# Optimization experiments

Hardware: AMD Instinct MI355X
Metric: run time of the kernel (lower is better)

## Reference

```python
import jax, jax.numpy as jnp
import numpy as np

NUM_HEADS = 16
H_SELF = 10  # hardcoded h in forward: first 10 heads self-attend, rest cross-attend
DIM = 1024
HEAD_DIM = DIM // NUM_HEADS
SCALE = HEAD_DIM ** -0.5


def _qkv(x, Wqkv):
    # x: [B, N, C] -> q, k, v each [B, H, N, hd]
    B, N, C = x.shape
    qkv = (x @ Wqkv).reshape(B, N, 3, NUM_HEADS, C // NUM_HEADS).transpose(2, 0, 3, 1, 4)
    return qkv[0], qkv[1], qkv[2]


def _attn(q, k, v):
    # q,k,v: [B, h, N, d]
    scores = jnp.einsum('bhqd,bhkd->bhqk', q, k) * SCALE
    probs = jax.nn.softmax(scores, axis=-1)  # attn_drop_ratio = 0.0
    return jnp.einsum('bhqk,bhkd->bhqd', probs, v)


def _proj(xa, xb, Wproj, bproj):
    # xa: [B, 10, N, d], xb: [B, 6, N, d] -> [B, N, C]
    B = xa.shape[0]
    N = xa.shape[2]
    x = jnp.concatenate([xa, xb], axis=1).transpose(0, 2, 1, 3).reshape(B, N, DIM)
    return x @ Wproj + bproj  # proj_drop_ratio = 0.0


def setup_inputs() -> dict:
    key = jax.random.key(0)
    k0, k1, k2, k3 = jax.random.split(key, 4)
    B, N, C = 16, 577, DIM
    x1 = jax.random.normal(k0, (B, N, C), dtype=jnp.float32)
    x2 = jax.random.normal(k1, (B, N, C), dtype=jnp.float32)
    # nn.Linear(dim, dim*3, bias=False): store as [C, 3C] so y = x @ W
    Wqkv = jax.random.normal(k2, (C, 3 * C), dtype=jnp.float32) * 0.02
    # nn.Linear(dim, dim) has bias by default
    Wproj = jax.random.normal(k3, (C, C), dtype=jnp.float32) * 0.02
    bproj = jnp.zeros((C,), dtype=jnp.float32)
    return {"x1": x1, "x2": x2, "Wqkv": Wqkv, "Wproj": Wproj, "bproj": bproj}


def reference(x1, x2, Wqkv, Wproj, bproj):
    q1, k1, v1 = _qkv(x1, Wqkv)
    q2, k2, v2 = _qkv(x2, Wqkv)
    h = H_SELF
    x11 = _attn(q1[:, :h], k1[:, :h], v1[:, :h])  # self-attn branch of x1
    x12 = _attn(q1[:, h:], k2[:, h:], v2[:, h:])  # cross: q from x1, kv from x2
    x22 = _attn(q2[:, :h], k2[:, :h], v2[:, :h])  # self-attn branch of x2
    x21 = _attn(q2[:, h:], k1[:, h:], v1[:, h:])  # cross: q from x2, kv from x1
    out1 = _proj(x11, x12, Wproj, bproj)
    out2 = _proj(x22, x21, Wproj, bproj)
    return (out1, out2)
```

## Files before the change

### kernel.cpp

```cpp
#include <hip/hip_runtime.h>
#include <hip/hip_bf16.h>
#include <stdint.h>
#include <math.h>

typedef __attribute__((ext_vector_type(8))) short bf16x8;
typedef __attribute__((ext_vector_type(4))) float f32x4;
typedef __attribute__((ext_vector_type(8))) unsigned short ushort8;
typedef __attribute__((ext_vector_type(4))) unsigned int uint4v;
typedef __attribute__((ext_vector_type(2))) unsigned int uint2v;

#define NTOK   9232
#define MROWS  18464
#define MPAD   18560
#define NPADV  640
#define QSCALE 0.18033688011112042f

__device__ __forceinline__ uint16_t f2b(float f) {
  uint32_t u = __builtin_bit_cast(uint32_t, f);
  u += 0x7fffu + ((u >> 16) & 1u);
  return (uint16_t)(u >> 16);
}

__device__ __forceinline__ uint32_t packbf(float lo, float hi) {
  return (uint32_t)f2b(lo) | ((uint32_t)f2b(hi) << 16);
}

__device__ __forceinline__ f32x4 mfma16(bf16x8 a, bf16x8 b, f32x4 c) {
  return __builtin_amdgcn_mfma_f32_16x16x32_bf16(a, b, c, 0, 0, 0);
}

__device__ __forceinline__ void gl_lds16(const void* g, void* l) {
  __builtin_amdgcn_global_load_lds(
      (const __attribute__((address_space(1))) uint32_t*)g,
      (__attribute__((address_space(3))) uint32_t*)l, 16, 0, 0);
}

__global__ void convert_x_kernel(const float* __restrict__ x1,
                                 const float* __restrict__ x2,
                                 uint16_t* __restrict__ Xb) {
  const size_t stride = (size_t)gridDim.x * blockDim.x;
  const size_t total8 = (size_t)MPAD * 1024 / 8;
  for (size_t i = (size_t)blockIdx.x * blockDim.x + threadIdx.x; i < total8; i += stride) {
    const size_t e = i * 8;
    const size_t row = e >> 10;
    ushort8 ov;
    if (row < (size_t)MROWS) {
      const float* src = (row < (size_t)NTOK) ? (x1 + e) : (x2 + (e - (size_t)NTOK * 1024));
      float4 a = *(const float4*)(src);
      float4 b = *(const float4*)(src + 4);
      ov[0] = f2b(a.x); ov[1] = f2b(a.y); ov[2] = f2b(a.z); ov[3] = f2b(a.w);
      ov[4] = f2b(b.x); ov[5] = f2b(b.y); ov[6] = f2b(b.z); ov[7] = f2b(b.w);
    } else {
      ov = (ushort8)0;
    }
    *(ushort8*)(Xb + e) = ov;
  }
}

__global__ void transw_kernel(const float* __restrict__ in, uint16_t* __restrict__ out,
                              int R, int Cc) {
  __shared__ float t[32][33];
  const int r0 = blockIdx.x * 32, c0 = blockIdx.y * 32;
  const int tr = threadIdx.x >> 5, tc = threadIdx.x & 31;
#pragma unroll
  for (int i = 0; i < 4; ++i)
    t[tr + i * 8][tc] = in[(size_t)(r0 + tr + i * 8) * Cc + c0 + tc];
  __syncthreads();
#pragma unroll
  for (int i = 0; i < 4; ++i) {
    const int orow = c0 + tr + i * 8;
    out[(size_t)orow * R + r0 + tc] = f2b(t[tc][tr + i * 8]);
  }
}

__global__ void zero_vpad_kernel(uint16_t* __restrict__ Vtb) {
  const int idx = blockIdx.x * 256 + threadIdx.x;
  for (int i = idx; i < 32768 * 8; i += 256 * 256) {
    const int p = i >> 3;
    const int ch = i & 7;
    *(ushort8*)(Vtb + (size_t)p * NPADV + 576 + ch * 8) = (ushort8)0;
  }
}

#define GEMM_TRI_SETUP                                                         \
  const int srow4 = tt >> 2;                                        \
  const int schunk = tt & 3;                         \
  const int swc = schunk ^ ((srow4 >> 1) & 3);                                 \
  const int crs = (c >> 1) & 3;                                                \
  char* aL = (char*)As3;                                                       \
  char* bL = (char*)Bs3;                                                       \
  auto SA = [&](int buf, int t) {                                              \
    _Pragma("unroll")                                                          \
    for (int i = 0; i < 2; ++i) {                                              \
      const int row = i * 64 + srow4;                                          \
      gl_lds16(aG + (size_t)row * 2048 + t * 64 + (swc << 4),                  \
               aL + buf * 8192 + row * 64 + (schunk << 4));                    \
    }                                                                          \
  };                                                                           \
  auto SB = [&](int buf, int t) {                                              \
    _Pragma("unroll")                                                          \
    for (int i = 0; i < 2; ++i) {                                              \
      const int row = i * 64 + srow4;                                          \
      gl_lds16(bG + (size_t)row * 2048 + t * 64 + (swc << 4),                  \
               bL + buf * 8192 + row * 64 + (schunk << 4));                    \
    }                                                                          \
  };                                                                           \
  auto LDA = [&](int buf, int mi) -> bf16x8 {                                  \
    const int r = wm * 64 + mi * 16 + c;                                       \
    return *(const bf16x8*)(aL + buf * 8192 + r * 64 + ((g ^ crs) << 4));      \
  };                                                                           \
  auto LDB = [&](int buf, int ni) -> bf16x8 {                                  \
    const int r = wn * 64 + ni * 16 + c;                                       \
    return *(const bf16x8*)(bL + buf * 8192 + r * 64 + ((g ^ crs) << 4));      \
  };

#define G_MFMA_BLOCK(BR)                                                       \
  {                                                                            \
    bf16x8 b0 = LDB(BR, 0), b1 = LDB(BR, 1);                                   \
    bf16x8 b2 = LDB(BR, 2), b3 = LDB(BR, 3);                                   \
    __builtin_amdgcn_s_setprio(1);                                             \
    _Pragma("unroll")                                                          \
    for (int mi = 0; mi < 4; ++mi) {                                           \
      const bf16x8 a0 = LDA(BR, mi);                                           \
      acc[mi][0] = mfma16(a0, b0, acc[mi][0]);                                 \
      acc[mi][1] = mfma16(a0, b1, acc[mi][1]);                                 \
      acc[mi][2] = mfma16(a0, b2, acc[mi][2]);                                 \
      acc[mi][3] = mfma16(a0, b3, acc[mi][3]);                                 \
    }                                                                          \
    __builtin_amdgcn_s_setprio(0);                                             \
  }

#define G_ITER_S(T, BR, BS)                                                    \
  {                                                                            \
    asm volatile("s_waitcnt vmcnt(4)" ::: "memory");                           \
    __builtin_amdgcn_s_barrier();                                              \
    __builtin_amdgcn_sched_barrier(0);                                         \
    SA(BS, (T) + 2); SB(BS, (T) + 2);                                          \
    G_MFMA_BLOCK(BR)                                                           \
  }

#define G_ITER_N(BR, VM)                                                       \
  {                                                                            \
    asm volatile("s_waitcnt vmcnt(" #VM ")" ::: "memory");                     \
    __builtin_amdgcn_s_barrier();                                              \
    __builtin_amdgcn_sched_barrier(0);                                         \
    G_MFMA_BLOCK(BR)                                                           \
  }

#define GEMM_TRI_KLOOP                                                         \
  GEMM_TRI_SETUP                                                               \
  SA(0, 0); SB(0, 0); SA(1, 1); SB(1, 1);                                      \
  for (int j = 0; j < 10; ++j) {                                               \
    const int t3 = j * 3;                                                      \
    G_ITER_S(t3, 0, 2)                                                         \
    G_ITER_S(t3 + 1, 1, 0)                                                     \
    G_ITER_S(t3 + 2, 2, 1)                                                     \
  }                                                                            \
  G_ITER_N(0, 4)                                                               \
  G_ITER_N(1, 0)

__global__ __launch_bounds__(256, 3) void gemm_qkv_kernel(
    const uint16_t* __restrict__ A, const uint16_t* __restrict__ Bt,
    uint16_t* __restrict__ Qb, uint16_t* __restrict__ Kb, uint16_t* __restrict__ Vtb) {
  __shared__ uint16_t As3[3][4096];
  __shared__ uint16_t Bs3[3][4096];
  const int tt = threadIdx.x;
  const int w = tt >> 6, l = tt & 63;
  const int c = l & 15, g = l >> 4;
  const int wgid = blockIdx.x;
  const int work = (wgid & 7) * 435 + (wgid >> 3);
  int bm, bn;
  {
    const int stripe = work / 144;
    if (stripe >= 24) { bm = 144; bn = work - 24 * 144; }
    else {
      const int r2 = work % 144;
      const int st8 = r2 / 48, r3 = r2 % 48;
      bm = stripe * 6 + r3 % 6;
      bn = st8 * 8 + r3 / 6;
    }
  }
  const int wm = w >> 1, wn = w & 1;
  f32x4 acc[4][4] = {};
  const char* aG = (const char*)(A + (size_t)bm * 128 * 1024);
  const char* bG = (const char*)(Bt + (size_t)bn * 128 * 1024);

  GEMM_TRI_KLOOP

  const int sArea = bn >> 3;
#pragma unroll
  for (int mi = 0; mi < 4; ++mi) {
#pragma unroll
    for (int r = 0; r < 4; ++r) {
      const int R = bm * 128 + wm * 64 + mi * 16 + g * 4 + r;
      if (R >= MROWS) continue;
      const int src = (R >= NTOK) ? 1 : 0;
      const int rr = R - src * NTOK;
      const int bb = rr / 577;
      const int nn = rr - bb * 577;
#pragma unroll
      for (int ni = 0; ni < 4; ++ni) {
        const int C = bn * 128 + wn * 64 + ni * 16 + c;
        const int c10 = C & 1023;
        const int hh = c10 >> 6, dd = c10 & 63;
        const size_t bh = ((size_t)src * 16 + bb) * 16 + hh;
        const float v = acc[mi][ni][r];
        if (sArea == 0)
          Qb[(bh * 577 + nn) * 64 + dd] = f2b(v * QSCALE);
        else if (sArea == 1)
          Kb[(bh * 577 + nn) * 64 + dd] = f2b(v);
        else
          Vtb[(bh * 64 + dd) * NPADV + nn] = f2b(v);
      }
    }
  }
}

#define KVB 64
#define ATT_NT 10
__global__ __launch_bounds__(256, 2) void attn_kernel(
    const uint16_t* __restrict__ Qb, const uint16_t* __restrict__ Kb,
    const uint16_t* __restrict__ Vtb, uint16_t* __restrict__ O) {
  __shared__ __align__(128) char smem[73728];
  const int tid = threadIdx.x;
  const int w = tid >> 6, l = tid & 63;
  const int c = l & 15, g = l >> 4;
  const int bid = blockIdx.x;
  const int qc = bid & 1;
  const int p = bid >> 1;
  const int h = p & 15, b = (p >> 4) & 15, o = p >> 8;
  const int kvsrc = (h < 10) ? o : (1 - o);
  const uint16_t* qp = Qb + (((size_t)o * 16 + b) * 16 + h) * 577 * 64;
  const uint16_t* kp = Kb + (((size_t)kvsrc * 16 + b) * 16 + h) * 577 * 64;
  const uint16_t* vp = Vtb + (((size_t)kvsrc * 16 + b) * 16 + h) * 64 * NPADV;

  const int qbase = qc * 320 + w * 80;

  const int sub = l >> 3;
  const int colEl = (((l & 7) ^ sub) << 3);
  char* KsA = smem;
  char* VsA = smem + 16384;
  char* Pb  = smem + 32768 + w * 10240;
  const int rs = (c & 7) << 4;

  bf16x8 Qf[5][2];
#pragma unroll
  for (int qt = 0; qt < 5; ++qt) {
    const int qrow = min(qbase + qt * 16 + c, 576);
    const uint16_t* qr = qp + (size_t)qrow * 64 + g * 8;
    Qf[qt][0] = *(const bf16x8*)(qr);
    Qf[qt][1] = *(const bf16x8*)(qr + 32);
  }

  f32x4 acc[4][5] = {};
  float m_run[5] = {-3.0e38f, -3.0e38f, -3.0e38f, -3.0e38f, -3.0e38f};
  float l_run[5] = {0.f, 0.f, 0.f, 0.f, 0.f};

  auto STAGE = [&](int buf, int kv0) {
#pragma unroll
    for (int i = 0; i < 2; ++i) {
      const int j = w * 2 + i;
      const int row = j * 8 + sub;
      const int gk = min(kv0 + row, 576);
      gl_lds16(kp + (size_t)gk * 64 + colEl, KsA + buf * 8192 + j * 1024 + l * 16);
      gl_lds16(vp + (size_t)row * NPADV + kv0 + colEl, VsA + buf * 8192 + j * 1024 + l * 16);
    }
  };

  STAGE(0, 0);
  __syncthreads();

  for (int t = 0; t < ATT_NT; ++t) {
    if (t < ATT_NT - 1) STAGE((t + 1) & 1, (t + 1) * KVB);
    {
      const char* Kt = KsA + (t & 1) * 8192;
      const char* Vt = VsA + (t & 1) * 8192;
      bf16x8 Kf[4][2];
#pragma unroll
      for (int kt = 0; kt < 4; ++kt) {
        const char* kr = Kt + (kt * 16 + c) * 128;
        Kf[kt][0] = *(const bf16x8*)(kr + ((g * 16) ^ rs));
        Kf[kt][1] = *(const bf16x8*)(kr + ((64 + g * 16) ^ rs));
      }
      float alpha_[5];
#pragma unroll
      for (int qt = 0; qt < 5; ++qt) {
        f32x4 s[4];
#pragma unroll
        for (int kt = 0; kt < 4; ++kt) {
          f32x4 z = {0.f, 0.f, 0.f, 0.f};
          z = mfma16(Kf[kt][0], Qf[qt][0], z);
          z = mfma16(Kf[kt][1], Qf[qt][1], z);
          s[kt] = z;
        }
        if (t == ATT_NT - 1) {
#pragma unroll
          for (int kt = 0; kt < 4; ++kt)
#pragma unroll
            for (int r = 0; r < 4; ++r) {
              if (kt == 0 && r == 0) { if (g > 0) s[kt][r] = -3.0e38f; }
              else s[kt][r] = -3.0e38f;
            }
        }
        float mt = s[0][0];
#pragma unroll
        for (int kt = 0; kt < 4; ++kt)
#pragma unroll
          for (int r = 0; r < 4; ++r) mt = fmaxf(mt, s[kt][r]);
        mt = fmaxf(mt, __shfl_xor(mt, 16));
        mt = fmaxf(mt, __shfl_xor(mt, 32));
        const float mnew = fmaxf(m_run[qt], mt);
        const float al = exp2f(m_run[qt] - mnew);
        m_run[qt] = mnew;
        alpha_[qt] = al;
        float lt = 0.f;
#pragma unroll
        for (int kt = 0; kt < 4; ++kt)
#pragma unroll
          for (int r = 0; r < 4; ++r) {
            const float pv = exp2f(s[kt][r] - mnew);
            s[kt][r] = pv;
            lt += pv;
          }
        lt += __shfl_xor(lt, 16);
        lt += __shfl_xor(lt, 32);
        l_run[qt] = l_run[qt] * al + lt;
        const int rowOff = (qt * 16 + c) * 128;
#pragma unroll
        for (int kt = 0; kt < 4; ++kt) {
          const uint2v pw = {packbf(s[kt][0], s[kt][1]), packbf(s[kt][2], s[kt][3])};
          *(uint2v*)(Pb + rowOff + ((kt * 32 + g * 8) ^ rs)) = pw;
        }
      }
#pragma unroll
      for (int dt = 0; dt < 4; ++dt)
#pragma unroll
        for (int qt = 0; qt < 5; ++qt)
#pragma unroll
          for (int r = 0; r < 4; ++r) acc[dt][qt][r] *= alpha_[qt];
      bf16x8 pf[5][2];
#pragma unroll
      for (int qt = 0; qt < 5; ++qt) {
        const char* pr = Pb + (qt * 16 + c) * 128;
        pf[qt][0] = *(const bf16x8*)(pr + ((g * 16) ^ rs));
        pf[qt][1] = *(const bf16x8*)(pr + ((64 + g * 16) ^ rs));
      }
#pragma unroll
      for (int dt = 0; dt < 4; ++dt) {
        const char* vr = Vt + (dt * 16 + c) * 128;
        const bf16x8 v0 = *(const bf16x8*)(vr + ((g * 16) ^ rs));
        const bf16x8 v1 = *(const bf16x8*)(vr + ((64 + g * 16) ^ rs));
#pragma unroll
        for (int qt = 0; qt < 5; ++qt) {
          acc[dt][qt] = mfma16(v0, pf[qt][0], acc[dt][qt]);
          acc[dt][qt] = mfma16(v1, pf[qt][1], acc[dt][qt]);
        }
      }
    }
    __syncthreads();
  }

  {
#pragma unroll
    for (int qt = 0; qt < 5; ++qt) {
      const float inv = 1.0f / l_run[qt];
      const int rowOff = (qt * 16 + c) * 128;
#pragma unroll
      for (int dt = 0; dt < 4; ++dt) {
        const uint2v pw = {packbf(acc[dt][qt][0] * inv, acc[dt][qt][1] * inv),
                           packbf(acc[dt][qt][2] * inv, acc[dt][qt][3] * inv)};
        *(uint2v*)(Pb + rowOff + ((dt * 32 + g * 8) ^ rs)) = pw;
      }
    }
    const size_t obase = ((size_t)o * NTOK + (size_t)b * 577) * 1024 + h * 64;
#pragma unroll
    for (int pass = 0; pass < 10; ++pass) {
      const int row = pass * 8 + (l >> 3);
      const int tok = qbase + row;
      const uint4v vv = *(const uint4v*)(Pb + row * 128 + (((l & 7) * 16) ^ ((row & 7) << 4)));
      if (tok <= 576)
        *(uint4v*)(O + obase + (size_t)tok * 1024 + (l & 7) * 8) = vv;
    }
  }
}

__global__ __launch_bounds__(256, 3) void gemm_proj_kernel(
    const uint16_t* __restrict__ A, const uint16_t* __restrict__ Bt,
    const float* __restrict__ bias, float* __restrict__ out) {
  __shared__ uint16_t As3[3][4096];
  __shared__ uint16_t Bs3[3][4096];
  const int tt = threadIdx.x;
  const int w = tt >> 6, l = tt & 63;
  const int c = l & 15, g = l >> 4;
  const int wgid = blockIdx.x;
  const int work = (wgid & 7) * 145 + (wgid >> 3);
  int bm, bn;
  {
    const int stripe = work / 48;
    if (stripe >= 24) { bm = 144; bn = work - 24 * 48; }
    else { const int r3 = work % 48; bm = stripe * 6 + r3 % 6; bn = r3 / 6; }
  }
  const int wm = w >> 1, wn = w & 1;
  f32x4 acc[4][4] = {};
  const char* aG = (const char*)(A + (size_t)bm * 128 * 1024);
  const char* bG = (const char*)(Bt + (size_t)bn * 128 * 1024);

  GEMM_TRI_KLOOP

#pragma unroll
  for (int mi = 0; mi < 4; ++mi) {
#pragma unroll
    for (int r = 0; r < 4; ++r) {
      const int R = bm * 128 + wm * 64 + mi * 16 + g * 4 + r;
      if (R >= MROWS) continue;
#pragma unroll
      for (int ni = 0; ni < 4; ++ni) {
        const int C = bn * 128 + wn * 64 + ni * 16 + c;
        out[(size_t)R * 1024 + C] = acc[mi][ni][r] + bias[C];
      }
    }
  }
}

extern "C" void kernel_launch(void* const* d_in, const int* in_sizes, int n_in,
                              void* d_out, int out_size, void* d_ws, size_t ws_size,
                              hipStream_t stream) {
  (void)in_sizes; (void)n_in; (void)out_size; (void)ws_size;
  const float* x1    = (const float*)d_in[0];
  const float* x2    = (const float*)d_in[1];
  const float* Wqkv  = (const float*)d_in[2];
  const float* Wproj = (const float*)d_in[3];
  const float* bproj = (const float*)d_in[4];
  float* out = (float*)d_out;

  char* ws = (char*)d_ws;
  size_t off = 0;
  auto alloc = [&](size_t bytes) -> char* {
    char* p = ws + off;
    off += (bytes + 255) & ~(size_t)255;
    return p;
  };
  uint16_t* Xb     = (uint16_t*)alloc((size_t)MPAD * 1024 * 2);
  uint16_t* Wqkvt  = (uint16_t*)alloc((size_t)3072 * 1024 * 2);
  uint16_t* Wprojt = (uint16_t*)alloc((size_t)1024 * 1024 * 2);
  uint16_t* Qb     = (uint16_t*)alloc((size_t)512 * 577 * 64 * 2);
  uint16_t* Kb     = (uint16_t*)alloc((size_t)512 * 577 * 64 * 2);
  uint16_t* Vtb    = (uint16_t*)alloc((size_t)512 * 64 * NPADV * 2);

  zero_vpad_kernel<<<256, 256, 0, stream>>>(Vtb);
  convert_x_kernel<<<2048, 256, 0, stream>>>(x1, x2, Xb);
  transw_kernel<<<dim3(32, 96), 256, 0, stream>>>(Wqkv, Wqkvt, 1024, 3072);
  transw_kernel<<<dim3(32, 32), 256, 0, stream>>>(Wproj, Wprojt, 1024, 1024);
  gemm_qkv_kernel<<<3480, 256, 0, stream>>>(Xb, Wqkvt, Qb, Kb, Vtb);
  attn_kernel<<<1024, 256, 0, stream>>>(Qb, Kb, Vtb, Xb );
  gemm_proj_kernel<<<1160, 256, 0, stream>>>(Xb, Wprojt, bproj, out);
}
```

Baseline: 389.0 us.

## Enlarge QKV GEMM tile to 256x256 with 512-thread workgroups

```diff
diff --git a/kernel.cpp b/kernel.cpp
--- a/kernel.cpp
+++ b/kernel.cpp
@@ -11,7 +11,7 @@
 
 #define NTOK   9232
 #define MROWS  18464
-#define MPAD   18560
+#define MPAD   18688
 #define NPADV  640
 #define QSCALE 0.18033688011112042f
 
@@ -79,6 +79,141 @@
     const int p = i >> 3;
     const int ch = i & 7;
     *(ushort8*)(Vtb + (size_t)p * NPADV + 576 + ch * 8) = (ushort8)0;
+  }
+}
+
+#define G256_SETUP                                                             \
+  const int srow = tt >> 2;                                        \
+  const int schunk = tt & 3;                         \
+  const int swc = schunk ^ ((srow >> 1) & 3);                                  \
+  const int crs = (c >> 1) & 3;                                                \
+  char* aL = (char*)As3;                                                       \
+  char* bL = (char*)Bs3;                                                       \
+  auto SA = [&](int buf, int t) {                                              \
+    _Pragma("unroll")                                                          \
+    for (int i = 0; i < 2; ++i) {                                              \
+      const int row = i * 128 + srow;                                          \
+      gl_lds16(aG + (size_t)row * 2048 + t * 64 + (swc << 4),                  \
+               aL + buf * 16384 + row * 64 + (schunk << 4));                   \
+    }                                                                          \
+  };                                                                           \
+  auto SB = [&](int buf, int t) {                                              \
+    _Pragma("unroll")                                                          \
+    for (int i = 0; i < 2; ++i) {                                              \
+      const int row = i * 128 + srow;                                          \
+      gl_lds16(bG + (size_t)row * 2048 + t * 64 + (swc << 4),                  \
+               bL + buf * 16384 + row * 64 + (schunk << 4));                   \
+    }                                                                          \
+  };                                                                           \
+  auto LDA = [&](int buf, int mi) -> bf16x8 {                                  \
+    const int r = wm * 128 + mi * 16 + c;                                      \
+    return *(const bf16x8*)(aL + buf * 16384 + r * 64 + ((g ^ crs) << 4));     \
+  };                                                                           \
+  auto LDB = [&](int buf, int ni) -> bf16x8 {                                  \
+    const int r = wn * 64 + ni * 16 + c;                                       \
+    return *(const bf16x8*)(bL + buf * 16384 + r * 64 + ((g ^ crs) << 4));     \
+  };
+
+#define G256_MFMA_BLOCK(BR)                                                    \
+  {                                                                            \
+    bf16x8 b0 = LDB(BR, 0), b1 = LDB(BR, 1);                                   \
+    bf16x8 b2 = LDB(BR, 2), b3 = LDB(BR, 3);                                   \
+    __builtin_amdgcn_s_setprio(1);                                             \
+    _Pragma("unroll")                                                          \
+    for (int mi = 0; mi < 8; ++mi) {                                           \
+      const bf16x8 a0 = LDA(BR, mi);                                           \
+      acc[mi][0] = mfma16(a0, b0, acc[mi][0]);                                 \
+      acc[mi][1] = mfma16(a0, b1, acc[mi][1]);                                 \
+      acc[mi][2] = mfma16(a0, b2, acc[mi][2]);                                 \
+      acc[mi][3] = mfma16(a0, b3, acc[mi][3]);                                 \
+    }                                                                          \
+    __builtin_amdgcn_s_setprio(0);                                             \
+  }
+
+#define G256_ITER_S(T, BR, BS)                                                 \
+  {                                                                            \
+    asm volatile("s_waitcnt vmcnt(4)" ::: "memory");                           \
+    __builtin_amdgcn_s_barrier();                                              \
+    __builtin_amdgcn_sched_barrier(0);                                         \
+    SA(BS, (T) + 2); SB(BS, (T) + 2);                                          \
+    G256_MFMA_BLOCK(BR)                                                        \
+  }
+
+#define G256_ITER_N(BR, VM)                                                    \
+  {                                                                            \
+    asm volatile("s_waitcnt vmcnt(" #VM ")" ::: "memory");                     \
+    __builtin_amdgcn_s_barrier();                                              \
+    __builtin_amdgcn_sched_barrier(0);                                         \
+    G256_MFMA_BLOCK(BR)                                                        \
+  }
+
+#define G256_KLOOP                                                             \
+  G256_SETUP                                                                   \
+  SA(0, 0); SB(0, 0); SA(1, 1); SB(1, 1);                                      \
+  for (int j = 0; j < 10; ++j) {                                               \
+    const int t3 = j * 3;                                                      \
+    G256_ITER_S(t3, 0, 2)                                                      \
+    G256_ITER_S(t3 + 1, 1, 0)                                                  \
+    G256_ITER_S(t3 + 2, 2, 1)                                                  \
+  }                                                                            \
+  G256_ITER_N(0, 4)                                                            \
+  G256_ITER_N(1, 0)
+
+__global__ __launch_bounds__(512, 1) void gemm_qkv_kernel(
+    const uint16_t* __restrict__ A, const uint16_t* __restrict__ Bt,
+    uint16_t* __restrict__ Qb, uint16_t* __restrict__ Kb, uint16_t* __restrict__ Vtb) {
+  __shared__ uint16_t As3[3][8192];
+  __shared__ uint16_t Bs3[3][8192];
+  const int tt = threadIdx.x;
+  const int w = tt >> 6, l = tt & 63;
+  const int c = l & 15, g = l >> 4;
+  const int wm = w >> 2, wn = w & 3;
+  const int orig = blockIdx.x;
+  const int xcd = orig & 7, sub8 = orig >> 3;
+  const int work = (xcd < 4 ? xcd * 110 : 440 + (xcd - 4) * 109) + sub8;
+  int bm, bn;
+  {
+    const int stripe = work / 36;
+    if (stripe >= 24) { bm = 72; bn = work - 864; }
+    else {
+      const int r2 = work % 36;
+      const int bg = r2 / 12, r3 = r2 % 12;
+      bm = stripe * 3 + r3 % 3;
+      bn = bg * 4 + r3 / 3;
+    }
+  }
+  f32x4 acc[8][4] = {};
+  const char* aG = (const char*)(A + (size_t)bm * 256 * 1024);
+  const char* bG = (const char*)(Bt + (size_t)bn * 256 * 1024);
+
+  G256_KLOOP
+
+  const int sArea = bn >> 2;
+#pragma unroll
+  for (int mi = 0; mi < 8; ++mi) {
+#pragma unroll
+    for (int r = 0; r < 4; ++r) {
+      const int R = bm * 256 + wm * 128 + mi * 16 + g * 4 + r;
+      if (R >= MROWS) continue;
+      const int src = (R >= NTOK) ? 1 : 0;
+      const int rr = R - src * NTOK;
+      const int bb = rr / 577;
+      const int nn = rr - bb * 577;
+#pragma unroll
+      for (int ni = 0; ni < 4; ++ni) {
+        const int C = bn * 256 + wn * 64 + ni * 16 + c;
+        const int c10 = C & 1023;
+        const int hh = c10 >> 6, dd = c10 & 63;
+        const size_t bh = ((size_t)src * 16 + bb) * 16 + hh;
+        const float v = acc[mi][ni][r];
+        if (sArea == 0)
+          Qb[(bh * 577 + nn) * 64 + dd] = f2b(v * QSCALE);
+        else if (sArea == 1)
+          Kb[(bh * 577 + nn) * 64 + dd] = f2b(v);
+        else
+          Vtb[(bh * 64 + dd) * NPADV + nn] = f2b(v);
+      }
+    }
   }
 }
 
@@ -159,63 +294,6 @@
   G_ITER_N(0, 4)                                                               \
   G_ITER_N(1, 0)
 
-__global__ __launch_bounds__(256, 3) void gemm_qkv_kernel(
-    const uint16_t* __restrict__ A, const uint16_t* __restrict__ Bt,
-    uint16_t* __restrict__ Qb, uint16_t* __restrict__ Kb, uint16_t* __restrict__ Vtb) {
-  __shared__ uint16_t As3[3][4096];
-  __shared__ uint16_t Bs3[3][4096];
-  const int tt = threadIdx.x;
-  const int w = tt >> 6, l = tt & 63;
-  const int c = l & 15, g = l >> 4;
-  const int wgid = blockIdx.x;
-  const int work = (wgid & 7) * 435 + (wgid >> 3);
-  int bm, bn;
-  {
-    const int stripe = work / 144;
-    if (stripe >= 24) { bm = 144; bn = work - 24 * 144; }
-    else {
-      const int r2 = work % 144;
-      const int st8 = r2 / 48, r3 = r2 % 48;
-      bm = stripe * 6 + r3 % 6;
-      bn = st8 * 8 + r3 / 6;
-    }
-  }
-  const int wm = w >> 1, wn = w & 1;
-  f32x4 acc[4][4] = {};
-  const char* aG = (const char*)(A + (size_t)bm * 128 * 1024);
-  const char* bG = (const char*)(Bt + (size_t)bn * 128 * 1024);
-
-  GEMM_TRI_KLOOP
-
-  const int sArea = bn >> 3;
-#pragma unroll
-  for (int mi = 0; mi < 4; ++mi) {
-#pragma unroll
-    for (int r = 0; r < 4; ++r) {
-      const int R = bm * 128 + wm * 64 + mi * 16 + g * 4 + r;
-      if (R >= MROWS) continue;
-      const int src = (R >= NTOK) ? 1 : 0;
-      const int rr = R - src * NTOK;
-      const int bb = rr / 577;
-      const int nn = rr - bb * 577;
-#pragma unroll
-      for (int ni = 0; ni < 4; ++ni) {
-        const int C = bn * 128 + wn * 64 + ni * 16 + c;
-        const int c10 = C & 1023;
-        const int hh = c10 >> 6, dd = c10 & 63;
-        const size_t bh = ((size_t)src * 16 + bb) * 16 + hh;
-        const float v = acc[mi][ni][r];
-        if (sArea == 0)
-          Qb[(bh * 577 + nn) * 64 + dd] = f2b(v * QSCALE);
-        else if (sArea == 1)
-          Kb[(bh * 577 + nn) * 64 + dd] = f2b(v);
-        else
-          Vtb[(bh * 64 + dd) * NPADV + nn] = f2b(v);
-      }
-    }
-  }
-}
-
 #define KVB 64
 #define ATT_NT 10
 __global__ __launch_bounds__(256, 2) void attn_kernel(
@@ -451,7 +529,7 @@
   convert_x_kernel<<<2048, 256, 0, stream>>>(x1, x2, Xb);
   transw_kernel<<<dim3(32, 96), 256, 0, stream>>>(Wqkv, Wqkvt, 1024, 3072);
   transw_kernel<<<dim3(32, 32), 256, 0, stream>>>(Wproj, Wprojt, 1024, 1024);
-  gemm_qkv_kernel<<<3480, 256, 0, stream>>>(Xb, Wqkvt, Qb, Kb, Vtb);
+  gemm_qkv_kernel<<<876, 512, 0, stream>>>(Xb, Wqkvt, Qb, Kb, Vtb);
   attn_kernel<<<1024, 256, 0, stream>>>(Qb, Kb, Vtb, Xb );
   gemm_proj_kernel<<<1160, 256, 0, stream>>>(Xb, Wprojt, bproj, out);
 }
```

After: 388.3 us. Within noise of the previous version (-0.2%).
